# Optimization experiments

Hardware: AMD Instinct MI355X
Metric: run time of the kernel (lower is better)

## Reference

```python
import jax, jax.numpy as jnp
from jax import lax
import numpy as np

B, T, H = 256, 1000, 256
V_TH = 0.5  # spike threshold from source: spike(v - 0.5)


def setup_inputs() -> dict:
    key = jax.random.key(0)
    x = jax.random.normal(key, (B, T, H), dtype=jnp.float32)
    decay_logit = jnp.ones((H,), dtype=jnp.float32)  # nn.initializers.constant(1.0)
    return {"x": x, "decay_logit": decay_logit}


def reference(x, decay_logit):
    # LIF recurrence: v = v * sigmoid(decay) * (1 - z_prev) + x_t ; z = heaviside(v - 0.5)
    dtype = x.dtype
    Bv, Tv, Hv = x.shape
    decay = jax.nn.sigmoid(decay_logit).astype(dtype)  # [H]

    def step(carry, xt):
        v, z = carry                      # [B,H] each
        v = v * decay * (1.0 - z) + xt    # decay gated by previous spike (soft reset)
        z = (v - V_TH > 0).astype(dtype)  # spike
        return (v, z), z

    init = (jnp.zeros((Bv, Hv), dtype), jnp.zeros((Bv, Hv), dtype))
    x_tbh = jnp.swapaxes(x, 0, 1)         # [T,B,H] for scan over time
    _, spk = lax.scan(step, init, x_tbh)  # spk: [T,B,H]
    return jnp.swapaxes(spk, 0, 1)        # [B,T,H]
```

## Files before the change

kernel.cpp:

```cpp
#include <hip/hip_runtime.h>
#include <math.h>

constexpr int T_LEN  = 1000;
constexpr int H_DIM  = 256;
constexpr int BATCH  = 20;
constexpr int NBATCH = T_LEN / BATCH;
constexpr int RING   = 3;
constexpr int DEPTH  = 2;
constexpr int RPW    = BATCH / 4;

typedef const __attribute__((address_space(1))) float g_f;
typedef __attribute__((address_space(3))) float l_f;

__global__ __launch_bounds__(256)
void lif_fwd(const float* __restrict__ x,
             const float* __restrict__ decay_logit,
             float* __restrict__ out)
{
#pragma clang fp contract(off)
    __shared__ float X[RING][BATCH][H_DIM];

    const int tid  = threadIdx.x;
    const int wv   = tid >> 6;
    const int lane = tid & 63;
    const int b    = blockIdx.x;

    const float* __restrict__ xrow = x   + (size_t)b * (T_LEN * H_DIM);
    float* __restrict__       orow = out + (size_t)b * (T_LEN * H_DIM) + tid;

    const float d = (float)(1.0 / (1.0 + exp(-(double)decay_logit[tid])));
    float v = 0.0f;
    bool  z = false;

    auto stage = [&](int bt) {
        const float* gsrc = xrow + (size_t)bt * (BATCH * H_DIM)
                                 + (size_t)(wv * RPW) * H_DIM + lane * 4;
        l_f* lds = (l_f*)&X[bt % RING][wv * RPW][0];
#pragma unroll
        for (int r = 0; r < RPW; ++r)
            __builtin_amdgcn_global_load_lds((g_f*)(gsrc + r * H_DIM),
                                             lds + r * H_DIM, 16, 0, 0);
    };

    stage(0);
    stage(1);

#pragma unroll 1
    for (int j = 0; j < NBATCH; ++j) {
        if (j + DEPTH < NBATCH) stage(j + DEPTH);

        if (j == 0) { asm volatile("s_waitcnt vmcnt(10)" ::: "memory"); }
        else        { asm volatile("s_waitcnt vmcnt(30)" ::: "memory"); }
        __builtin_amdgcn_sched_barrier(0);
        __builtin_amdgcn_s_barrier();

        const float(*Xj)[H_DIM] = X[j % RING];
        float* op = orow + (size_t)j * (BATCH * H_DIM);
#pragma unroll
        for (int t = 0; t < BATCH; ++t) {
            float xt = Xj[t][tid];
            float vd = v * d;
            float vg = z ? 0.0f : vd;
            v = vg + xt;
            z = (v > 0.5f);
            __builtin_nontemporal_store(z ? 1.0f : 0.0f, op + (size_t)t * H_DIM);
        }

        __builtin_amdgcn_s_barrier();
    }
}

extern "C" void kernel_launch(void* const* d_in, const int* in_sizes, int n_in,
                              void* d_out, int out_size, void* d_ws, size_t ws_size,
                              hipStream_t stream)
{
    const float* x  = (const float*)d_in[0];
    const float* dl = (const float*)d_in[1];
    float*       o  = (float*)d_out;

    const int B = in_sizes[0] / (T_LEN * H_DIM);
    lif_fwd<<<B, 256, 0, stream>>>(x, dl, o);
}
```

Baseline: 94.78 us.

## Give each wave a private LDS ring and drop block barriers

The shared staging buffer is split per wave, so each wave loads only the 64 hidden columns it consumes. That removes both s_barrier calls per batch, and each wave now synchronises only through its own vmcnt waits. The ring is deepened from 3 to 7 slots with a prefetch depth of 6, which keeps more global loads in flight. LDS use grows, which may lower occupancy, and correctness now depends on the hand-set vmcnt counts matching the per-wave load and store counts.

```diff
diff --git a/kernel.cpp b/kernel.cpp
--- a/kernel.cpp
+++ b/kernel.cpp
@@ -1,13 +1,13 @@
 #include <hip/hip_runtime.h>
 #include <math.h>
 
-constexpr int T_LEN  = 1000;
-constexpr int H_DIM  = 256;
-constexpr int BATCH  = 20;
-constexpr int NBATCH = T_LEN / BATCH;
-constexpr int RING   = 3;
-constexpr int DEPTH  = 2;
-constexpr int RPW    = BATCH / 4;
+constexpr int T_LEN = 1000;
+constexpr int H_DIM = 256;
+constexpr int SROWS = 20;
+constexpr int NSLOT = T_LEN / SROWS;
+constexpr int RING  = 7;
+constexpr int DEPTH = 6;
+constexpr int GPS   = SROWS / 4;
 
 typedef const __attribute__((address_space(1))) float g_f;
 typedef __attribute__((address_space(3))) float l_f;
@@ -18,56 +18,65 @@
              float* __restrict__ out)
 {
 #pragma clang fp contract(off)
-    __shared__ float X[RING][BATCH][H_DIM];
+    __shared__ float X[4][RING][SROWS][64];
 
     const int tid  = threadIdx.x;
     const int wv   = tid >> 6;
     const int lane = tid & 63;
     const int b    = blockIdx.x;
 
-    const float* __restrict__ xrow = x   + (size_t)b * (T_LEN * H_DIM);
-    float* __restrict__       orow = out + (size_t)b * (T_LEN * H_DIM) + tid;
+    const float* __restrict__ xrow  = x   + (size_t)b * (T_LEN * H_DIM);
+    float* __restrict__       obase = out + (size_t)b * (T_LEN * H_DIM)
+                                          + (wv << 6) + lane;
 
     const float d = (float)(1.0 / (1.0 + exp(-(double)decay_logit[tid])));
     float v = 0.0f;
     bool  z = false;
 
-    auto stage = [&](int bt) {
-        const float* gsrc = xrow + (size_t)bt * (BATCH * H_DIM)
-                                 + (size_t)(wv * RPW) * H_DIM + lane * 4;
-        l_f* lds = (l_f*)&X[bt % RING][wv * RPW][0];
+    const size_t srcofs = (size_t)(lane >> 4) * H_DIM + (wv << 6) + ((lane & 15) << 2);
+
+    auto stage = [&](int s) {
+        const float* gsrc = xrow + (size_t)s * (SROWS * H_DIM) + srcofs;
+        l_f* lds = (l_f*)&X[wv][s % RING][0][0];
 #pragma unroll
-        for (int r = 0; r < RPW; ++r)
-            __builtin_amdgcn_global_load_lds((g_f*)(gsrc + r * H_DIM),
-                                             lds + r * H_DIM, 16, 0, 0);
+        for (int g = 0; g < GPS; ++g)
+            __builtin_amdgcn_global_load_lds((g_f*)(gsrc + (size_t)(4 * g) * H_DIM),
+                                             lds + g * (4 * 64), 16, 0, 0);
     };
 
-    stage(0);
-    stage(1);
+#pragma unroll
+    for (int s = 0; s < DEPTH; ++s) stage(s);
 
+#define LIF_ITER(WCNT)                                                        \
+    {                                                                         \
+        asm volatile("s_waitcnt vmcnt(" #WCNT ")" ::: "memory");              \
+        __builtin_amdgcn_sched_barrier(0);                                    \
+        if (j + DEPTH < NSLOT) stage(j + DEPTH);                              \
+        const float(*Xs)[64] = X[wv][j % RING];                               \
+        float* op = obase + (size_t)j * (SROWS * H_DIM);                      \
+        _Pragma("unroll")                                                     \
+        for (int t = 0; t < SROWS; ++t) {                                     \
+            float xt = Xs[t][lane];           \
+            float vd = v * d;                 \
+            float vg = z ? 0.0f : vd;         \
+            v = vg + xt;                      \
+            z = (v > 0.5f);                   \
+            __builtin_nontemporal_store(z ? 1.0f : 0.0f,                      \
+                                        op + (size_t)t * H_DIM);              \
+        }                                                                     \
+    }
+
+    {
+        int j = 0;
+        LIF_ITER(25)
+    }
+    {
+        int j = 1;
+        LIF_ITER(40)
+    }
 #pragma unroll 1
-    for (int j = 0; j < NBATCH; ++j) {
-        if (j + DEPTH < NBATCH) stage(j + DEPTH);
-
-        if (j == 0) { asm volatile("s_waitcnt vmcnt(10)" ::: "memory"); }
-        else        { asm volatile("s_waitcnt vmcnt(30)" ::: "memory"); }
-        __builtin_amdgcn_sched_barrier(0);
-        __builtin_amdgcn_s_barrier();
-
-        const float(*Xj)[H_DIM] = X[j % RING];
-        float* op = orow + (size_t)j * (BATCH * H_DIM);
-#pragma unroll
-        for (int t = 0; t < BATCH; ++t) {
-            float xt = Xj[t][tid];
-            float vd = v * d;
-            float vg = z ? 0.0f : vd;
-            v = vg + xt;
-            z = (v > 0.5f);
-            __builtin_nontemporal_store(z ? 1.0f : 0.0f, op + (size_t)t * H_DIM);
-        }
-
-        __builtin_amdgcn_s_barrier();
-    }
+    for (int j = 2; j < NSLOT; ++j) LIF_ITER(62)
+#undef LIF_ITER
 }
 
 extern "C" void kernel_launch(void* const* d_in, const int* in_sizes, int n_in,
```

After: 81.38 us. 1.16x faster.

## Split block into compute and I/O warps with LDS-staged spike output

Applied to the files above, without the earlier changes.

Doubles the block to 512 threads. Four compute waves run the recurrence and write spikes into a double-buffered LDS tile. Four producer/consumer waves prefetch input via global_load_lds with a deeper ring (5 slots, depth 4) and flush the spike tiles as 16-byte vector nontemporal stores. The aim is to take global memory traffic off the serial recurrence path and widen the output stores, at the cost of more LDS, extra barriers and hand-tuned vmcnt accounting.

```diff
diff --git a/kernel.cpp b/kernel.cpp
--- a/kernel.cpp
+++ b/kernel.cpp
@@ -1,72 +1,98 @@
 #include <hip/hip_runtime.h>
 #include <math.h>
 
-constexpr int T_LEN  = 1000;
-constexpr int H_DIM  = 256;
-constexpr int BATCH  = 20;
-constexpr int NBATCH = T_LEN / BATCH;
-constexpr int RING   = 3;
-constexpr int DEPTH  = 2;
-constexpr int RPW    = BATCH / 4;
+constexpr int T_LEN = 1000;
+constexpr int H_DIM = 256;
+constexpr int SROWS = 20;
+constexpr int NSLOT = T_LEN / SROWS;
+constexpr int RING  = 5;
+constexpr int DEPTH = 4;
+constexpr int RPIO  = SROWS / 4;
 
 typedef const __attribute__((address_space(1))) float g_f;
 typedef __attribute__((address_space(3))) float l_f;
+typedef float v4f __attribute__((ext_vector_type(4)));
 
-__global__ __launch_bounds__(256)
+__global__ __launch_bounds__(512)
 void lif_fwd(const float* __restrict__ x,
              const float* __restrict__ decay_logit,
              float* __restrict__ out)
 {
 #pragma clang fp contract(off)
-    __shared__ float X[RING][BATCH][H_DIM];
+    __shared__ float X[RING][SROWS][H_DIM];
+    __shared__ float Z[2][SROWS][H_DIM];
 
     const int tid  = threadIdx.x;
     const int wv   = tid >> 6;
     const int lane = tid & 63;
     const int b    = blockIdx.x;
 
-    const float* __restrict__ xrow = x   + (size_t)b * (T_LEN * H_DIM);
-    float* __restrict__       orow = out + (size_t)b * (T_LEN * H_DIM) + tid;
+    const float* __restrict__ xrow  = x   + (size_t)b * (T_LEN * H_DIM);
+    float* __restrict__       obase = out + (size_t)b * (T_LEN * H_DIM);
 
-    const float d = (float)(1.0 / (1.0 + exp(-(double)decay_logit[tid])));
-    float v = 0.0f;
-    bool  z = false;
+    if (wv < 4) {
+        const float d = (float)(1.0 / (1.0 + exp(-(double)decay_logit[tid])));
+        float v = 0.0f;
+        bool  z = false;
+#pragma unroll 1
+        for (int j = 0; j < NSLOT; ++j) {
+            __builtin_amdgcn_s_barrier();
+            const float(*Xs)[H_DIM] = X[j % RING];
+            float(*Zs)[H_DIM] = Z[j & 1];
+#pragma unroll
+            for (int t = 0; t < SROWS; ++t) {
+                float xt = Xs[t][tid];
+                float vd = v * d;
+                float vg = z ? 0.0f : vd;
+                v = vg + xt;
+                z = (v > 0.5f);
+                Zs[t][tid] = z ? 1.0f : 0.0f;
+            }
+            asm volatile("s_waitcnt lgkmcnt(0)" ::: "memory");
+            __builtin_amdgcn_sched_barrier(0);
+            __builtin_amdgcn_s_barrier();
+        }
+    } else {
+        const int w = wv - 4;
 
-    auto stage = [&](int bt) {
-        const float* gsrc = xrow + (size_t)bt * (BATCH * H_DIM)
-                                 + (size_t)(wv * RPW) * H_DIM + lane * 4;
-        l_f* lds = (l_f*)&X[bt % RING][wv * RPW][0];
+        auto stage = [&](int s) {
+            const float* gsrc = xrow + (size_t)s * (SROWS * H_DIM)
+                                     + (size_t)(w * RPIO) * H_DIM + lane * 4;
+            l_f* lds = (l_f*)&X[s % RING][w * RPIO][0];
 #pragma unroll
-        for (int r = 0; r < RPW; ++r)
-            __builtin_amdgcn_global_load_lds((g_f*)(gsrc + r * H_DIM),
-                                             lds + r * H_DIM, 16, 0, 0);
-    };
+            for (int r = 0; r < RPIO; ++r)
+                __builtin_amdgcn_global_load_lds((g_f*)(gsrc + (size_t)r * H_DIM),
+                                                 lds + r * H_DIM, 16, 0, 0);
+        };
+        auto flush = [&](int js) {
+            const float(*Zs)[H_DIM] = Z[js & 1];
+#pragma unroll
+            for (int r = 0; r < RPIO; ++r) {
+                v4f pk = *(const v4f*)&Zs[w * RPIO + r][lane * 4];
+                __builtin_nontemporal_store(pk,
+                    (v4f*)(obase + (size_t)(js * SROWS + w * RPIO + r) * H_DIM
+                                 + lane * 4));
+            }
+        };
 
-    stage(0);
-    stage(1);
+#pragma unroll
+        for (int s = 0; s < DEPTH; ++s) stage(s);
 
 #pragma unroll 1
-    for (int j = 0; j < NBATCH; ++j) {
-        if (j + DEPTH < NBATCH) stage(j + DEPTH);
-
-        if (j == 0) { asm volatile("s_waitcnt vmcnt(10)" ::: "memory"); }
-        else        { asm volatile("s_waitcnt vmcnt(30)" ::: "memory"); }
-        __builtin_amdgcn_sched_barrier(0);
-        __builtin_amdgcn_s_barrier();
-
-        const float(*Xj)[H_DIM] = X[j % RING];
-        float* op = orow + (size_t)j * (BATCH * H_DIM);
-#pragma unroll
-        for (int t = 0; t < BATCH; ++t) {
-            float xt = Xj[t][tid];
-            float vd = v * d;
-            float vg = z ? 0.0f : vd;
-            v = vg + xt;
-            z = (v > 0.5f);
-            __builtin_nontemporal_store(z ? 1.0f : 0.0f, op + (size_t)t * H_DIM);
+        for (int j = 0; j < NSLOT; ++j) {
+            if      (j < 2)  { asm volatile("s_waitcnt vmcnt(15)" ::: "memory"); }
+            else if (j < 4)  { asm volatile("s_waitcnt vmcnt(25)" ::: "memory"); }
+            else if (j == 4) { asm volatile("s_waitcnt vmcnt(30)" ::: "memory"); }
+            else             { asm volatile("s_waitcnt vmcnt(35)" ::: "memory"); }
+            __builtin_amdgcn_sched_barrier(0);
+            __builtin_amdgcn_s_barrier();
+            if (j + DEPTH < NSLOT) stage(j + DEPTH);
+            __builtin_amdgcn_sched_barrier(0);
+            if (j > 0) flush(j - 1);
+            __builtin_amdgcn_sched_barrier(0);
+            __builtin_amdgcn_s_barrier();
         }
-
-        __builtin_amdgcn_s_barrier();
+        flush(NSLOT - 1);
     }
 }
 
@@ -79,5 +105,5 @@
     float*       o  = (float*)d_out;
 
     const int B = in_sizes[0] / (T_LEN * H_DIM);
-    lif_fwd<<<B, 256, 0, stream>>>(x, dl, o);
+    lif_fwd<<<B, 512, 0, stream>>>(x, dl, o);
 }
```

Result: faster. 80.72 us (-14.8%).
